# Kernel optimization log

Measured on AMD Instinct MI355X. Metric: run time of the kernel, lower is better.

Reference implementation:

```python
import jax, jax.numpy as jnp
import numpy as np

NEG = -1e9

def _lstm(x, Wih, Whh, b):
    # x: [B,S,D]; PyTorch gate order i,f,g,o; Wih:[4H,D], Whh:[4H,H], b:[4H]
    B = x.shape[0]
    H = Whh.shape[1]
    def step(carry, xt):
        h, c = carry
        g = xt @ Wih.T + h @ Whh.T + b
        i, f, gg, o = jnp.split(g, 4, axis=-1)
        c = jax.nn.sigmoid(f) * c + jax.nn.sigmoid(i) * jnp.tanh(gg)
        h = jax.nn.sigmoid(o) * jnp.tanh(c)
        return (h, c), h
    init = (jnp.zeros((B, H), x.dtype), jnp.zeros((B, H), x.dtype))
    _, hs = jax.lax.scan(step, init, x.transpose(1, 0, 2))
    return hs.transpose(1, 0, 2)  # [B,S,H]

def _bilstm(x, Wih_f, Whh_f, b_f, Wih_b, Whh_b, b_b):
    fwd = _lstm(x, Wih_f, Whh_f, b_f)
    bwd = jnp.flip(_lstm(jnp.flip(x, 1), Wih_b, Whh_b, b_b), 1)
    return jnp.concatenate([fwd, bwd], axis=-1)

def _windowed_attention(h, attn_W, attn_b, window_size):
    # score(i,j) = W @ [h_i, h_j, h_i*h_j] + b, decomposed exactly:
    #   = h_i@w1 + h_j@w2 + (h_i*w3)@h_j + b, masked to |i-j| <= window
    S = h.shape[1]
    w1, w2, w3 = jnp.split(attn_W[0], 3)
    s1 = h @ w1                                   # [B,S]
    s2 = h @ w2                                   # [B,S]
    cross = jnp.einsum('bid,bjd->bij', h * w3, h)  # [B,S,S]
    scores = s1[:, :, None] + s2[:, None, :] + cross + attn_b[0]
    idx = jnp.arange(S)
    band = jnp.abs(idx[:, None] - idx[None, :]) <= window_size
    scores = jnp.where(band, scores, NEG)
    p = jax.nn.softmax(scores, axis=-1)
    return jnp.einsum('bij,bjd->bid', p, h)       # [B,S,H]

def _forward(x, lstm1_Wih_f, lstm1_Whh_f, lstm1_b_f, lstm1_Wih_b, lstm1_Whh_b, lstm1_b_b,
             fc1_W, fc1_b, attn_W, attn_b,
             lstm2_Wih_f, lstm2_Whh_f, lstm2_b_f, lstm2_Wih_b, lstm2_Whh_b, lstm2_b_b,
             l2_W1, l2_b1, l2_W2, l2_b2, l2_W3, l2_b3, window_size):
    # dropout layers are identity at inference
    lstm_out = _bilstm(x, lstm1_Wih_f, lstm1_Whh_f, lstm1_b_f,
                       lstm1_Wih_b, lstm1_Whh_b, lstm1_b_b)          # [B,S,768]
    h = lstm_out @ fc1_W.T + fc1_b                                    # [B,S,384]
    attn = _windowed_attention(h, attn_W, attn_b, window_size)        # [B,S,384]
    h_cat = jnp.concatenate([h, attn], axis=-1)                       # [B,S,768]
    lstm_out2 = _bilstm(h_cat, lstm2_Wih_f, lstm2_Whh_f, lstm2_b_f,
                        lstm2_Wih_b, lstm2_Whh_b, lstm2_b_b)          # [B,S,768]
    h2 = lstm_out2 @ fc1_W.T + fc1_b                                  # fc1 reused, as in source
    y = jax.nn.relu(h2 @ l2_W1.T + l2_b1)
    y = jax.nn.relu(y @ l2_W2.T + l2_b2)
    return y @ l2_W3.T + l2_b3                                        # [B,S,1]

def setup_inputs() -> dict:
    key = jax.random.key(0)
    ks = iter(jax.random.split(key, 32))
    D, H, B, S = 768, 384, 16, 1024
    sc = 0.02
    def rn(shape):
        return jax.random.normal(next(ks), shape, dtype=jnp.float32) * sc
    inp = {'x': jax.random.normal(next(ks), (B, S, D), dtype=jnp.float32)}
    for name in ('lstm1', 'lstm2'):
        inp[f'{name}_Wih_f'] = rn((4 * H, D)); inp[f'{name}_Whh_f'] = rn((4 * H, H))
        inp[f'{name}_b_f'] = rn((4 * H,))
        inp[f'{name}_Wih_b'] = rn((4 * H, D)); inp[f'{name}_Whh_b'] = rn((4 * H, H))
        inp[f'{name}_b_b'] = rn((4 * H,))
    inp['fc1_W'] = rn((H, D)); inp['fc1_b'] = rn((H,))
    inp['attn_W'] = rn((1, 3 * H)); inp['attn_b'] = rn((1,))
    inp['l2_W1'] = rn((256, H)); inp['l2_b1'] = rn((256,))
    inp['l2_W2'] = rn((96, 256)); inp['l2_b2'] = rn((96,))
    inp['l2_W3'] = rn((1, 96)); inp['l2_b3'] = rn((1,))
    inp['window_size'] = 32
    return inp

def reference(x, lstm1_Wih_f, lstm1_Whh_f, lstm1_b_f, lstm1_Wih_b, lstm1_Whh_b, lstm1_b_b,
              fc1_W, fc1_b, attn_W, attn_b,
              lstm2_Wih_f, lstm2_Whh_f, lstm2_b_f, lstm2_Wih_b, lstm2_Whh_b, lstm2_b_b,
              l2_W1, l2_b1, l2_W2, l2_b2, l2_W3, l2_b3, window_size):
    return _forward(x, lstm1_Wih_f, lstm1_Whh_f, lstm1_b_f, lstm1_Wih_b, lstm1_Whh_b, lstm1_b_b,
                    fc1_W, fc1_b, attn_W, attn_b,
                    lstm2_Wih_f, lstm2_Whh_f, lstm2_b_f, lstm2_Wih_b, lstm2_Whh_b, lstm2_b_b,
                    l2_W1, l2_b1, l2_W2, l2_b2, l2_W3, l2_b3, window_size)
```

## Files before the change

kernel.cpp:

```cpp
#include <hip/hip_runtime.h>
#include <hip/hip_bf16.h>
#include <hip/hip_fp16.h>
#include <type_traits>

#define S_LEN 1024
#define BATCH 16
#define HID   384
#define DIN   768

#define GRP 8
#define UPB 48
#define NTHR 384

__device__ __forceinline__ float sigf(float x)     { return 1.f/(1.f + __expf(-x)); }
__device__ __forceinline__ float tanhfast(float x) { return 1.f - 2.f/(__expf(2.f*x) + 1.f); }

__device__ __forceinline__ __half2 unpackh2(float f) {
    return __builtin_bit_cast(__half2, f);
}

typedef __attribute__((ext_vector_type(8))) _Float16 f16x8;
typedef __attribute__((ext_vector_type(4))) float f32x4;

__global__ void zero_kernel(unsigned long long* hx)
{
    int i = blockIdx.x * blockDim.x + threadIdx.x;
    if (i < 32*2*HID) hx[i] = 0ull;
}

__global__ void prep16(const float* __restrict__ wf, const float* __restrict__ wb,
                       __half* __restrict__ o)
{
    int i = blockIdx.x * 256 + threadIdx.x;
    if (i < 147456) {
        const float4 a = ((const float4*)wf)[i];
        const float4 b = ((const float4*)wb)[i];
        __half2* of = (__half2*)o;
        of[2*i]   = __halves2half2(__float2half(a.x), __float2half(a.y));
        of[2*i+1] = __halves2half2(__float2half(a.z), __float2half(a.w));
        __half2* ob = (__half2*)(o + 589824);
        ob[2*i]   = __halves2half2(__float2half(b.x), __float2half(b.y));
        ob[2*i+1] = __halves2half2(__float2half(b.z), __float2half(b.w));
    }
}

__global__ __launch_bounds__(256) void gemm_f16(
    const float* __restrict__ A, int ldA,
    const float* __restrict__ W,
    const float* __restrict__ bias,
    __hip_bfloat16* __restrict__ C, int ldC,
    int K)
{
    __shared__ char Al[128 * 128];
    __shared__ char Bl[128 * 128];
    const int tid  = threadIdx.x;
    const int m0   = blockIdx.x * 128;
    const int n0   = blockIdx.y * 128;
    const int wid  = tid >> 6, lane = tid & 63;
    const int wm   = (wid >> 1) * 64, wn = (wid & 1) * 64;
    const int fr   = lane & 15, fq = lane >> 4;

    f32x4 acc[4][4] = {};

    const int srow = tid >> 1;
    const int sseg = (tid & 1) * 32;

    for (int k0 = 0; k0 < K; k0 += 64) {
        {
            const float* ap = A + (size_t)(m0 + srow) * ldA + k0 + sseg;
            const float* wp = W + (size_t)(n0 + srow) * K   + k0 + sseg;
            _Float16 ta[32], tw[32];
            #pragma unroll
            for (int q = 0; q < 8; q++) {
                const float4 va = *(const float4*)(ap + q * 4);
                const float4 vw = *(const float4*)(wp + q * 4);
                ta[4*q+0] = (_Float16)va.x; ta[4*q+1] = (_Float16)va.y;
                ta[4*q+2] = (_Float16)va.z; ta[4*q+3] = (_Float16)va.w;
                tw[4*q+0] = (_Float16)vw.x; tw[4*q+1] = (_Float16)vw.y;
                tw[4*q+2] = (_Float16)vw.z; tw[4*q+3] = (_Float16)vw.w;
            }
            const int xr = (srow & 7) << 4;
            #pragma unroll
            for (int c = 0; c < 4; c++) {
                const int col = (sseg * 2 + c * 16) ^ xr;
                *(f16x8*)(Al + srow * 128 + col) = *(f16x8*)&ta[c * 8];
                *(f16x8*)(Bl + srow * 128 + col) = *(f16x8*)&tw[c * 8];
            }
        }
        __syncthreads();

        #pragma unroll
        for (int kc = 0; kc < 2; kc++) {
            f16x8 af[4], bf[4];
            #pragma unroll
            for (int mt = 0; mt < 4; mt++) {
                const int r = wm + mt * 16 + fr;
                af[mt] = *(const f16x8*)(Al + r * 128 + ((kc * 64 + fq * 16) ^ ((r & 7) << 4)));
            }
            #pragma unroll
            for (int nt = 0; nt < 4; nt++) {
                const int r = wn + nt * 16 + fr;
                bf[nt] = *(const f16x8*)(Bl + r * 128 + ((kc * 64 + fq * 16) ^ ((r & 7) << 4)));
            }
            #pragma unroll
            for (int mt = 0; mt < 4; mt++)
                #pragma unroll
                for (int nt = 0; nt < 4; nt++)
                    acc[mt][nt] = __builtin_amdgcn_mfma_f32_16x16x32_f16(
                        af[mt], bf[nt], acc[mt][nt], 0, 0, 0);
        }
        __syncthreads();
    }

    #pragma unroll
    for (int mt = 0; mt < 4; mt++) {
        #pragma unroll
        for (int nt = 0; nt < 4; nt++) {
            const int n = n0 + wn + nt * 16 + fr;
            const float bv = bias[n];
            #pragma unroll
            for (int j = 0; j < 4; j++) {
                const int m = m0 + wm + mt * 16 + fq * 4 + j;
                C[(size_t)m * ldC + n] = __float2bfloat16(acc[mt][nt][j] + bv);
            }
        }
    }
}

template<int RELU, typename OT>
__global__ __launch_bounds__(256) void gemm_nt(
    const float* __restrict__ A, int ldA,
    const float* __restrict__ W,
    const float* __restrict__ bias,
    OT* __restrict__ C, int ldC,
    int M, int N, int K)
{
    __shared__ float As[16][132];
    __shared__ float Ws[16][68];
    const int tid = threadIdx.x;
    const int m0 = blockIdx.x * 128;
    const int n0 = blockIdx.y * 64;
    const int tm = (tid & 15) * 8;
    const int tn = (tid >> 4) * 4;

    float acc[8][4];
    #pragma unroll
    for (int i = 0; i < 8; i++)
        #pragma unroll
        for (int j = 0; j < 4; j++) acc[i][j] = 0.f;

    const int lrow = tid >> 2;
    const int lk   = (tid & 3) * 4;

    for (int k0 = 0; k0 < K; k0 += 16) {
        #pragma unroll
        for (int p = 0; p < 2; p++) {
            const int r = lrow + p * 64;
            const float4 av = *(const float4*)(A + (size_t)(m0 + r) * ldA + k0 + lk);
            As[lk+0][r] = av.x; As[lk+1][r] = av.y; As[lk+2][r] = av.z; As[lk+3][r] = av.w;
        }
        {
            float4 wv = make_float4(0.f, 0.f, 0.f, 0.f);
            if (n0 + lrow < N) wv = *(const float4*)(W + (size_t)(n0 + lrow) * K + k0 + lk);
            Ws[lk+0][lrow] = wv.x; Ws[lk+1][lrow] = wv.y; Ws[lk+2][lrow] = wv.z; Ws[lk+3][lrow] = wv.w;
        }
        __syncthreads();
        #pragma unroll
        for (int k = 0; k < 16; k++) {
            const float4 a0 = *(const float4*)&As[k][tm];
            const float4 a1 = *(const float4*)&As[k][tm + 4];
            const float4 bv = *(const float4*)&Ws[k][tn];
            const float am[8] = {a0.x, a0.y, a0.z, a0.w, a1.x, a1.y, a1.z, a1.w};
            const float bb[4] = {bv.x, bv.y, bv.z, bv.w};
            #pragma unroll
            for (int i = 0; i < 8; i++)
                #pragma unroll
                for (int j = 0; j < 4; j++) acc[i][j] += am[i] * bb[j];
        }
        __syncthreads();
    }

    #pragma unroll
    for (int i = 0; i < 8; i++) {
        const int m = m0 + tm + i;
        #pragma unroll
        for (int j = 0; j < 4; j++) {
            const int n = n0 + tn + j;
            if (n < N) {
                float v = acc[i][j] + bias[n];
                if (RELU) v = fmaxf(v, 0.f);
                if constexpr (std::is_same_v<OT, __hip_bfloat16>)
                    C[(size_t)m * ldC + n] = __float2bfloat16(v);
                else
                    C[(size_t)m * ldC + n] = v;
            }
        }
    }
}

__global__ __launch_bounds__(NTHR) void lstm_scan(
    const __hip_bfloat16* __restrict__ gatesF, const __hip_bfloat16* __restrict__ gatesB,
    const __half* __restrict__ wh16,
    float* __restrict__ out, unsigned long long* hx_all, int epoch)
{
    __shared__ float hl[2][HID];

    const int blk = blockIdx.x;
    const int g   = blk & 31;
    const int m   = blk >> 5;
    const int dir = g >> 4;
    const int b   = g & 15;
    const int u0  = m * UPB;

    const __hip_bfloat16* gates = dir ? gatesB : gatesF;
    const __half* wh = wh16 + (size_t)dir * 589824;
    unsigned long long* hx = hx_all + g * (2 * HID);

    const int tid = threadIdx.x;
    const int rr  = tid >> 3;
    const int ss  = tid & 7;
    const int ug  = u0 + rr;
    const bool owner = (ss == 0);

    float c_state = 0.f;
    const unsigned tbase = (unsigned)epoch * 2048u;

    for (int t = 0; t < S_LEN; t++) {
        const int tt = dir ? (S_LEN - 1 - t) : t;

        float gx0 = 0.f, gx1 = 0.f, gx2 = 0.f, gx3 = 0.f;
        if (owner) {
            const __hip_bfloat16* gp = gates + ((size_t)(b * S_LEN + tt)) * (4 * HID) + ug;
            gx0 = __bfloat162float(gp[0]);
            gx1 = __bfloat162float(gp[HID]);
            gx2 = __bfloat162float(gp[2 * HID]);
            gx3 = __bfloat162float(gp[3 * HID]);
        }

        if (t == 0) {
            if (tid < 128) {
                hl[0][tid] = 0.f; hl[0][tid + 128] = 0.f; hl[0][tid + 256] = 0.f;
            }
        } else if (tid < 128) {
            const unsigned long long* src = hx + ((t + 1) & 1) * HID;
            float* dst = hl[t & 1];
            const unsigned tgt = tbase + (unsigned)t;
            int pend = 7;
            long guard = 0;
            do {
                if (pend & 1) {
                    const unsigned long long q = __hip_atomic_load(src + tid,
                        __ATOMIC_RELAXED, __HIP_MEMORY_SCOPE_AGENT);
                    if ((unsigned)(q >> 32) >= tgt) {
                        dst[tid] = __uint_as_float((unsigned)q); pend &= ~1;
                    }
                }
                if (pend & 2) {
                    const unsigned long long q = __hip_atomic_load(src + tid + 128,
                        __ATOMIC_RELAXED, __HIP_MEMORY_SCOPE_AGENT);
                    if ((unsigned)(q >> 32) >= tgt) {
                        dst[tid + 128] = __uint_as_float((unsigned)q); pend &= ~2;
                    }
                }
                if (pend & 4) {
                    const unsigned long long q = __hip_atomic_load(src + tid + 256,
                        __ATOMIC_RELAXED, __HIP_MEMORY_SCOPE_AGENT);
                    if ((unsigned)(q >> 32) >= tgt) {
                        dst[tid + 256] = __uint_as_float((unsigned)q); pend &= ~4;
                    }
                }
                if (!pend) break;
                __builtin_amdgcn_s_sleep(1);
            } while (++guard < (1L << 22));
        }
        __syncthreads();

        const float* hsl = hl[t & 1];
        float a0 = 0.f, a1 = 0.f, a2 = 0.f, a3 = 0.f;
        #pragma unroll
        for (int jj = 0; jj < 6; jj++) {
            const float4 h40 = *(const float4*)(hsl + ss * 8 + 64 * jj);
            const float4 h41 = *(const float4*)(hsl + ss * 8 + 64 * jj + 4);
            #pragma unroll
            for (int gt = 0; gt < 4; gt++) {
                const float4 wv = *(const float4*)(wh + ((size_t)(gt * HID + ug)) * HID + ss * 8 + 64 * jj);
                const __half2 p0 = unpackh2(wv.x), p1 = unpackh2(wv.y),
                              p2 = unpackh2(wv.z), p3 = unpackh2(wv.w);
                float s = __low2float(p0) * h40.x + __high2float(p0) * h40.y
                        + __low2float(p1) * h40.z + __high2float(p1) * h40.w
                        + __low2float(p2) * h41.x + __high2float(p2) * h41.y
                        + __low2float(p3) * h41.z + __high2float(p3) * h41.w;
                if (gt == 0) a0 += s;
                else if (gt == 1) a1 += s;
                else if (gt == 2) a2 += s;
                else a3 += s;
            }
        }
        a0 += __shfl_xor(a0, 1, 64); a0 += __shfl_xor(a0, 2, 64); a0 += __shfl_xor(a0, 4, 64);
        a1 += __shfl_xor(a1, 1, 64); a1 += __shfl_xor(a1, 2, 64); a1 += __shfl_xor(a1, 4, 64);
        a2 += __shfl_xor(a2, 1, 64); a2 += __shfl_xor(a2, 2, 64); a2 += __shfl_xor(a2, 4, 64);
        a3 += __shfl_xor(a3, 1, 64); a3 += __shfl_xor(a3, 2, 64); a3 += __shfl_xor(a3, 4, 64);

        if (owner) {
            const float ii = sigf(a0 + gx0);
            const float ff = sigf(a1 + gx1);
            const float gg = tanhfast(a2 + gx2);
            const float oo = sigf(a3 + gx3);
            c_state = ff * c_state + ii * gg;
            const float hn = oo * tanhfast(c_state);
            const unsigned long long pk =
                ((unsigned long long)(tbase + (unsigned)t + 1u) << 32) |
                (unsigned long long)__float_as_uint(hn);
            __hip_atomic_store(hx + (t & 1) * HID + ug, pk,
                               __ATOMIC_RELAXED, __HIP_MEMORY_SCOPE_AGENT);
            out[((size_t)(b * S_LEN + tt)) * (2 * HID) + dir * HID + ug] = hn;
        }
    }
}

__global__ __launch_bounds__(256) void attn_win(
    const float* __restrict__ hcat,
    const float* __restrict__ attnW,
    float* __restrict__ ocat,
    const int* __restrict__ wsz_p)
{
    __shared__ float q[HID];
    __shared__ float sc[96];
    __shared__ float p[96];
    const int blk = blockIdx.x;
    const int b = blk >> 10, i = blk & 1023;
    const int W = *wsz_p;
    const int jlo = max(i - W, 0), jhi = min(i + W, S_LEN - 1);
    const int nj = jhi - jlo + 1;
    const int tid = threadIdx.x;
    const float* hrow = hcat + (size_t)b * S_LEN * 768;

    if (tid < 96) {
        const float4 hv = *(const float4*)(hrow + (size_t)i * 768 + tid * 4);
        const float4 w3 = *(const float4*)(attnW + 768 + tid * 4);
        const float4 w2 = *(const float4*)(attnW + 384 + tid * 4);
        float4 r;
        r.x = hv.x*w3.x + w2.x; r.y = hv.y*w3.y + w2.y;
        r.z = hv.z*w3.z + w2.z; r.w = hv.w*w3.w + w2.w;
        *(float4*)(q + tid * 4) = r;
    }
    __syncthreads();

    const int wv = tid >> 6, lane = tid & 63;
    for (int jj = wv; jj < nj; jj += 4) {
        const float* hj = hrow + (size_t)(jlo + jj) * 768;
        float s = 0.f;
        #pragma unroll
        for (int c = 0; c < 6; c++) { const int d = lane + 64*c; s += q[d] * hj[d]; }
        #pragma unroll
        for (int st = 1; st < 64; st <<= 1) s += __shfl_xor(s, st, 64);
        if (lane == 0) sc[jj] = s;
    }
    __syncthreads();

    if (tid < 64) {
        float v1 = (tid < nj) ? sc[tid] : -3e38f;
        float v2 = (64 + tid < nj) ? sc[64 + tid] : -3e38f;
        float m = fmaxf(v1, v2);
        #pragma unroll
        for (int st = 1; st < 64; st <<= 1) m = fmaxf(m, __shfl_xor(m, st, 64));
        float e1 = (tid < nj) ? __expf(v1 - m) : 0.f;
        float e2 = (64 + tid < nj) ? __expf(v2 - m) : 0.f;
        float sum = e1 + e2;
        #pragma unroll
        for (int st = 1; st < 64; st <<= 1) sum += __shfl_xor(sum, st, 64);
        const float inv = 1.f / sum;
        if (tid < nj) p[tid] = e1 * inv;
        if (64 + tid < nj) p[64 + tid] = e2 * inv;
    }
    __syncthreads();

    if (tid < 192) {
        const int d = tid * 2;
        float s0 = 0.f, s1 = 0.f;
        for (int jj = 0; jj < nj; jj++) {
            const float* hj = hrow + (size_t)(jlo + jj) * 768 + d;
            const float pj = p[jj];
            s0 += pj * hj[0]; s1 += pj * hj[1];
        }
        float* o = ocat + (size_t)b * S_LEN * 768 + (size_t)i * 768 + 384 + d;
        o[0] = s0; o[1] = s1;
    }
}

__global__ __launch_bounds__(256) void final_dot(
    const float* __restrict__ y2, const float* __restrict__ W3,
    const float* __restrict__ b3, float* __restrict__ outp)
{
    __shared__ float w[96];
    const int tid = threadIdx.x;
    if (tid < 96) w[tid] = W3[tid];
    __syncthreads();
    const int r = blockIdx.x * 256 + tid;
    const float* row = y2 + (size_t)r * 96;
    float s = 0.f;
    #pragma unroll
    for (int c = 0; c < 24; c++) {
        const float4 v = ((const float4*)row)[c];
        s += v.x*w[c*4] + v.y*w[c*4+1] + v.z*w[c*4+2] + v.w*w[c*4+3];
    }
    outp[r] = s + b3[0];
}

extern "C" void kernel_launch(void* const* d_in, const int* in_sizes, int n_in,
                              void* d_out, int out_size, void* d_ws, size_t ws_size,
                              hipStream_t stream)
{
    const float* x        = (const float*)d_in[0];
    const float* l1_Wih_f = (const float*)d_in[1];
    const float* l1_Whh_f = (const float*)d_in[2];
    const float* l1_b_f   = (const float*)d_in[3];
    const float* l1_Wih_b = (const float*)d_in[4];
    const float* l1_Whh_b = (const float*)d_in[5];
    const float* l1_b_b   = (const float*)d_in[6];
    const float* l2_Wih_f = (const float*)d_in[7];
    const float* l2_Whh_f = (const float*)d_in[8];
    const float* l2_b_f   = (const float*)d_in[9];
    const float* l2_Wih_b = (const float*)d_in[10];
    const float* l2_Whh_b = (const float*)d_in[11];
    const float* l2_b_b   = (const float*)d_in[12];
    const float* fc1_W    = (const float*)d_in[13];
    const float* fc1_b    = (const float*)d_in[14];
    const float* attn_W   = (const float*)d_in[15];
    const float* w1       = (const float*)d_in[17];
    const float* b1       = (const float*)d_in[18];
    const float* w2       = (const float*)d_in[19];
    const float* b2       = (const float*)d_in[20];
    const float* w3       = (const float*)d_in[21];
    const float* b3       = (const float*)d_in[22];
    const int*   wsz      = (const int*)d_in[23];

    char* wsb = (char*)d_ws;
    __hip_bfloat16*     gF  = (__hip_bfloat16*)(wsb);
    __hip_bfloat16*     gB  = (__hip_bfloat16*)(wsb +  50331648);
    float*              seq = (float*)(wsb + 100663296);
    float*              hct = (float*)(wsb + 150994944);
    unsigned long long* hx  = (unsigned long long*)(wsb + 201326592);
    float*              h2  = (float*)(wsb);
    float*              y1  = (float*)(wsb +  50331648);
    float*              y2  = (float*)(wsb +  50331648 + 16777216);
    __half*             w16 = (__half*)hct;

    const int M = BATCH * S_LEN;
    dim3 tb(256);

    zero_kernel<<<dim3(96), tb, 0, stream>>>(hx);
    prep16<<<dim3(576), tb, 0, stream>>>(l1_Whh_f, l1_Whh_b, w16);
    gemm_f16<<<dim3(M/128, 12), tb, 0, stream>>>(x, DIN, l1_Wih_f, l1_b_f, gF, 1536, DIN);
    gemm_f16<<<dim3(M/128, 12), tb, 0, stream>>>(x, DIN, l1_Wih_b, l1_b_b, gB, 1536, DIN);
    lstm_scan<<<dim3(256), dim3(NTHR), 0, stream>>>(gF, gB, w16, seq, hx, 0);

    gemm_nt<0, float><<<dim3(M/128, 6), tb, 0, stream>>>(seq, 768, fc1_W, fc1_b, hct, 768, M, 384, 768);
    attn_win<<<dim3(M), tb, 0, stream>>>(hct, attn_W, hct, wsz);

    gemm_f16<<<dim3(M/128, 12), tb, 0, stream>>>(hct, 768, l2_Wih_f, l2_b_f, gF, 1536, 768);
    gemm_f16<<<dim3(M/128, 12), tb, 0, stream>>>(hct, 768, l2_Wih_b, l2_b_b, gB, 1536, 768);
    prep16<<<dim3(576), tb, 0, stream>>>(l2_Whh_f, l2_Whh_b, w16);
    lstm_scan<<<dim3(256), dim3(NTHR), 0, stream>>>(gF, gB, w16, seq, hx, 1);

    gemm_nt<0, float><<<dim3(M/128, 6), tb, 0, stream>>>(seq, 768, fc1_W, fc1_b, h2, 384, M, 384, 768);
    gemm_nt<1, float><<<dim3(M/128, 4), tb, 0, stream>>>(h2, 384, w1, b1, y1, 256, M, 256, 384);
    gemm_nt<1, float><<<dim3(M/128, 2), tb, 0, stream>>>(y1, 256, w2, b2, y2, 96, M, 96, 256);
    final_dot<<<dim3(M/256), tb, 0, stream>>>(y2, w3, b3, (float*)d_out);
}
```

Measured before the change: 6.198 ms.

## Fold fc1 into l2 first layer, use MFMA GEMM, prefetch recurrent weights

The second fc1 projection and the first l2 layer are collapsed into a single precomputed 256x768 matrix and bias, which removes one full GEMM and its intermediate buffer. The fc1 GEMMs now run on the f16 MFMA kernel, which gains ReLU and fp32-output template variants. In the LSTM scan, each step's recurrent weight loads are issued before the spin-wait on h, so their latency can hide behind synchronisation, at the cost of extra register pressure. The f16 path and the folded weights change numerics slightly.

```diff
diff --git a/kernel.cpp b/kernel.cpp
--- a/kernel.cpp
+++ b/kernel.cpp
@@ -44,11 +44,44 @@
     }
 }
 
+__global__ __launch_bounds__(256) void prep_wc(
+    const float* __restrict__ fc1W,
+    const float* __restrict__ fc1b,
+    const float* __restrict__ w1,
+    const float* __restrict__ b1,
+    float* __restrict__ Wc,
+    float* __restrict__ bc)
+{
+    __shared__ float wr[384];
+    const int n = blockIdx.x;
+    const int tid = threadIdx.x;
+    if (tid < 192) {
+        const float2 v = *(const float2*)(w1 + (size_t)n * 384 + tid * 2);
+        wr[tid*2] = v.x; wr[tid*2+1] = v.y;
+    }
+    __syncthreads();
+    float s0 = 0.f, s1 = 0.f, s2 = 0.f;
+    for (int j = 0; j < 384; j++) {
+        const float w = wr[j];
+        const float* fr = fc1W + (size_t)j * 768;
+        s0 += w * fr[tid]; s1 += w * fr[tid + 256]; s2 += w * fr[tid + 512];
+    }
+    Wc[(size_t)n*768 + tid]       = s0;
+    Wc[(size_t)n*768 + tid + 256] = s1;
+    Wc[(size_t)n*768 + tid + 512] = s2;
+    if (tid == 0) {
+        float s = b1[n];
+        for (int j = 0; j < 384; j++) s += wr[j] * fc1b[j];
+        bc[n] = s;
+    }
+}
+
+template<int RELU, typename OT>
 __global__ __launch_bounds__(256) void gemm_f16(
     const float* __restrict__ A, int ldA,
     const float* __restrict__ W,
     const float* __restrict__ bias,
-    __hip_bfloat16* __restrict__ C, int ldC,
+    OT* __restrict__ C, int ldC,
     int K)
 {
     __shared__ char Al[128 * 128];
@@ -121,7 +154,12 @@
             #pragma unroll
             for (int j = 0; j < 4; j++) {
                 const int m = m0 + wm + mt * 16 + fq * 4 + j;
-                C[(size_t)m * ldC + n] = __float2bfloat16(acc[mt][nt][j] + bv);
+                float v = acc[mt][nt][j] + bv;
+                if (RELU) v = fmaxf(v, 0.f);
+                if constexpr (std::is_same_v<OT, __hip_bfloat16>)
+                    C[(size_t)m * ldC + n] = __float2bfloat16(v);
+                else
+                    C[(size_t)m * ldC + n] = v;
             }
         }
     }
@@ -236,6 +274,18 @@
             gx2 = __bfloat162float(gp[2 * HID]);
             gx3 = __bfloat162float(gp[3 * HID]);
         }
+
+        float4 wpre[24];
+        #pragma unroll
+        for (int jj = 0; jj < 6; jj++)
+            #pragma unroll
+            for (int gt = 0; gt < 4; gt++)
+                wpre[jj * 4 + gt] = *(const float4*)(
+                    wh + ((size_t)(gt * HID + ug)) * HID + ss * 8 + 64 * jj);
+        #pragma unroll
+        for (int i = 0; i < 24; i++)
+            asm volatile("" : "+v"(wpre[i].x), "+v"(wpre[i].y),
+                              "+v"(wpre[i].z), "+v"(wpre[i].w));
 
         if (t == 0) {
             if (tid < 128) {
@@ -283,7 +333,7 @@
             const float4 h41 = *(const float4*)(hsl + ss * 8 + 64 * jj + 4);
             #pragma unroll
             for (int gt = 0; gt < 4; gt++) {
-                const float4 wv = *(const float4*)(wh + ((size_t)(gt * HID + ug)) * HID + ss * 8 + 64 * jj);
+                const float4 wv = wpre[jj * 4 + gt];
                 const __half2 p0 = unpackh2(wv.x), p1 = unpackh2(wv.y),
                               p2 = unpackh2(wv.z), p3 = unpackh2(wv.w);
                 float s = __low2float(p0) * h40.x + __high2float(p0) * h40.y
@@ -441,30 +491,31 @@
     float*              seq = (float*)(wsb + 100663296);
     float*              hct = (float*)(wsb + 150994944);
     unsigned long long* hx  = (unsigned long long*)(wsb + 201326592);
-    float*              h2  = (float*)(wsb);
+    __half*             w16 = (__half*)hct;
+    float*              Wc  = (float*)(wsb);
+    float*              bc  = (float*)(wsb + 786432);
     float*              y1  = (float*)(wsb +  50331648);
     float*              y2  = (float*)(wsb +  50331648 + 16777216);
-    __half*             w16 = (__half*)hct;
 
     const int M = BATCH * S_LEN;
     dim3 tb(256);
 
     zero_kernel<<<dim3(96), tb, 0, stream>>>(hx);
     prep16<<<dim3(576), tb, 0, stream>>>(l1_Whh_f, l1_Whh_b, w16);
-    gemm_f16<<<dim3(M/128, 12), tb, 0, stream>>>(x, DIN, l1_Wih_f, l1_b_f, gF, 1536, DIN);
-    gemm_f16<<<dim3(M/128, 12), tb, 0, stream>>>(x, DIN, l1_Wih_b, l1_b_b, gB, 1536, DIN);
+    gemm_f16<0, __hip_bfloat16><<<dim3(M/128, 12), tb, 0, stream>>>(x, DIN, l1_Wih_f, l1_b_f, gF, 1536, DIN);
+    gemm_f16<0, __hip_bfloat16><<<dim3(M/128, 12), tb, 0, stream>>>(x, DIN, l1_Wih_b, l1_b_b, gB, 1536, DIN);
     lstm_scan<<<dim3(256), dim3(NTHR), 0, stream>>>(gF, gB, w16, seq, hx, 0);
 
-    gemm_nt<0, float><<<dim3(M/128, 6), tb, 0, stream>>>(seq, 768, fc1_W, fc1_b, hct, 768, M, 384, 768);
+    gemm_f16<0, float><<<dim3(M/128, 3), tb, 0, stream>>>(seq, 768, fc1_W, fc1_b, hct, 768, 768);
     attn_win<<<dim3(M), tb, 0, stream>>>(hct, attn_W, hct, wsz);
 
-    gemm_f16<<<dim3(M/128, 12), tb, 0, stream>>>(hct, 768, l2_Wih_f, l2_b_f, gF, 1536, 768);
-    gemm_f16<<<dim3(M/128, 12), tb, 0, stream>>>(hct, 768, l2_Wih_b, l2_b_b, gB, 1536, 768);
+    gemm_f16<0, __hip_bfloat16><<<dim3(M/128, 12), tb, 0, stream>>>(hct, 768, l2_Wih_f, l2_b_f, gF, 1536, 768);
+    gemm_f16<0, __hip_bfloat16><<<dim3(M/128, 12), tb, 0, stream>>>(hct, 768, l2_Wih_b, l2_b_b, gB, 1536, 768);
     prep16<<<dim3(576), tb, 0, stream>>>(l2_Whh_f, l2_Whh_b, w16);
     lstm_scan<<<dim3(256), dim3(NTHR), 0, stream>>>(gF, gB, w16, seq, hx, 1);
 
-    gemm_nt<0, float><<<dim3(M/128, 6), tb, 0, stream>>>(seq, 768, fc1_W, fc1_b, h2, 384, M, 384, 768);
-    gemm_nt<1, float><<<dim3(M/128, 4), tb, 0, stream>>>(h2, 384, w1, b1, y1, 256, M, 256, 384);
+    prep_wc<<<dim3(256), tb, 0, stream>>>(fc1_W, fc1_b, w1, b1, Wc, bc);
+    gemm_f16<1, float><<<dim3(M/128, 2), tb, 0, stream>>>(seq, 768, Wc, bc, y1, 256, 768);
     gemm_nt<1, float><<<dim3(M/128, 2), tb, 0, stream>>>(y1, 256, w2, b2, y2, 96, M, 96, 256);
     final_dot<<<dim3(M/256), tb, 0, stream>>>(y2, w3, b3, (float*)d_out);
 }
```

Result: slower. 7.320 ms (+18.1%).
